# Optimization experiments

Hardware: AMD Instinct MI355X
Metric: run time of the kernel (lower is better)

The kernel has to match this reference:

```python
import jax, jax.numpy as jnp
import numpy as np

N = 100000   # nodes
E = 1600000  # edges (before self loops)
IN = 128     # input feature dim
H = 64       # hidden dim (single head GAT)
OUT = 2      # classifier output
NEG_SLOPE = 0.2


def setup_inputs() -> dict:
    key = jax.random.key(0)
    ks = jax.random.split(key, 14)
    s_in = 1.0 / np.sqrt(IN)
    s_h = 1.0 / np.sqrt(H)
    return {
        "x": jax.random.normal(ks[0], (N, IN), jnp.float32),
        "edge_index": jax.random.randint(ks[1], (2, E), 0, N, dtype=jnp.int64),
        # layer 0: in_ch -> hidden
        "W0": jax.random.normal(ks[2], (IN, H), jnp.float32) * s_in,
        "asrc0": jax.random.normal(ks[3], (H,), jnp.float32) * s_h,
        "adst0": jax.random.normal(ks[4], (H,), jnp.float32) * s_h,
        "b0": jnp.zeros((H,), jnp.float32),
        # layers 1..2: hidden -> hidden (stacked)
        "Ws": jax.random.normal(ks[5], (2, H, H), jnp.float32) * s_h,
        "asrcs": jax.random.normal(ks[6], (2, H), jnp.float32) * s_h,
        "adsts": jax.random.normal(ks[7], (2, H), jnp.float32) * s_h,
        "bs": jnp.zeros((2, H), jnp.float32),
        # classifier
        "Wc": jax.random.normal(ks[8], (H, OUT), jnp.float32) * s_h,
        "bc": jnp.zeros((OUT,), jnp.float32),
    }


def _gat_conv(x, W, a_src, a_dst, b, src, dst):
    """Single-head PyG GATConv (add_self_loops already applied to src/dst)."""
    h = x @ W                                   # [N, H]
    logit_s = h @ a_src                         # [N]
    logit_d = h @ a_dst                         # [N]
    e = jax.nn.leaky_relu(logit_s[src] + logit_d[dst], NEG_SLOPE)  # [E']
    # segment softmax over destination neighborhoods
    m = jax.ops.segment_max(e, dst, num_segments=N)                # [N]
    p = jnp.exp(e - m[dst])                                        # [E']
    denom = jax.ops.segment_sum(p, dst, num_segments=N)            # [N]
    alpha = p / (denom[dst] + 1e-16)                               # [E']
    out = jax.ops.segment_sum(alpha[:, None] * h[src], dst, num_segments=N)
    return out + b


def reference(x, edge_index, W0, asrc0, adst0, b0, Ws, asrcs, adsts, bs, Wc, bc):
    # PyG GATConv default add_self_loops=True
    loops = jnp.arange(N, dtype=edge_index.dtype)
    src = jnp.concatenate([edge_index[0], loops])
    dst = jnp.concatenate([edge_index[1], loops])

    h = jax.nn.relu(_gat_conv(x, W0, asrc0, adst0, b0, src, dst))
    for i in range(2):  # remaining num_layers-1 = 2 layers
        h = jax.nn.relu(_gat_conv(h, Ws[i], asrcs[i], adsts[i], bs[i], src, dst))
    # dropout is identity in eval mode
    return h @ Wc + bc
```

## Files before the change

kernel.cpp:

```cpp
#include <hip/hip_runtime.h>
#include <hip/hip_bf16.h>
#include <math.h>

#define NNODES 100000
#define NEDGES 1600000
#define EPLUS  (NEDGES + NNODES)
#define INF    128
#define HF     64
#define NEG_SLOPE 0.2f

#define CHUNK  4096
#define NCH    416
#define K1SH   10
#define NBK    98
#define HTLEN  (NBK * NCH)

__device__ __forceinline__ void edge_at(const int* __restrict__ ei, int i, int& s, int& d) {
    if (i < NEDGES) { s = ei[i]; d = ei[NEDGES + i]; } else { s = d = i - NEDGES; }
}

__global__ __launch_bounds__(256) void k_p1hist(const int* __restrict__ ei, int* __restrict__ hT) {
    __shared__ int h[NBK];
    const int c = blockIdx.x, t = threadIdx.x;
    if (t < NBK) h[t] = 0;
    __syncthreads();
    #pragma unroll
    for (int j = 0; j < CHUNK / 256; ++j) {
        int i = c * CHUNK + j * 256 + t;
        if (i < EPLUS) {
            int d = (i < NEDGES) ? ei[NEDGES + i] : (i - NEDGES);
            atomicAdd(&h[d >> K1SH], 1);
        }
    }
    __syncthreads();
    if (t < NBK) hT[t * NCH + c] = h[t];
}

__global__ __launch_bounds__(1024) void k_p2scan(int* __restrict__ hT, int* __restrict__ roff) {
    __shared__ int wsum[16], wpre[16];
    __shared__ int carry;
    const int t = threadIdx.x, lane = t & 63, w = t >> 6;
    if (t == 0) carry = 0;
    __syncthreads();
    const int len4 = HTLEN / 4;
    for (int base4 = 0; base4 < len4; base4 += 1024) {
        int idx4 = base4 + t;
        int4 a = make_int4(0, 0, 0, 0);
        if (idx4 < len4) a = ((const int4*)hT)[idx4];
        int s = a.x + a.y + a.z + a.w;
        int inc = s;
        #pragma unroll
        for (int o = 1; o < 64; o <<= 1) { int u = __shfl_up(inc, o); if (lane >= o) inc += u; }
        if (lane == 63) wsum[w] = inc;
        __syncthreads();
        if (t < 16) {
            int v = wsum[t], iv = v;
            #pragma unroll
            for (int o = 1; o < 16; o <<= 1) { int u = __shfl_up(iv, o); if (t >= o) iv += u; }
            wpre[t] = iv - v;
        }
        __syncthreads();
        int cl = carry;
        int excl = inc - s + wpre[w] + cl;
        if (idx4 < len4) {
            int4 e; e.x = excl; e.y = e.x + a.x; e.z = e.y + a.y; e.w = e.z + a.z;
            ((int4*)hT)[idx4] = e;
        }
        __syncthreads();
        if (t == 1023) carry = cl + wpre[15] + wsum[15];
        __syncthreads();
    }
    if (t == 0) roff[NNODES] = EPLUS;
}

__global__ __launch_bounds__(256) void k_p3part(const int* __restrict__ ei,
        const int* __restrict__ hT, int* __restrict__ pairs) {
    __shared__ int cur[NBK];
    const int c = blockIdx.x, t = threadIdx.x;
    if (t < NBK) cur[t] = hT[t * NCH + c];
    __syncthreads();
    #pragma unroll
    for (int j = 0; j < CHUNK / 256; ++j) {
        int i = c * CHUNK + j * 256 + t;
        if (i < EPLUS) {
            int s, d; edge_at(ei, i, s, d);
            int pos = atomicAdd(&cur[d >> K1SH], 1);
            pairs[pos] = (s << K1SH) | (d & 1023);
        }
    }
}

__global__ __launch_bounds__(512) void k_p4local(const int* __restrict__ hT,
        const int* __restrict__ pairs, int* __restrict__ roff, int* __restrict__ csr) {
    __shared__ int cnt[1024], woffl[1024];
    __shared__ int wsum[8], wpre[8];
    const int k = blockIdx.x, t = threadIdx.x, lane = t & 63, w = t >> 6;
    const int rstart = hT[k * NCH];
    const int rend   = (k + 1 < NBK) ? hT[(k + 1) * NCH] : EPLUS;
    cnt[t] = 0; cnt[t + 512] = 0;
    __syncthreads();
    for (int i = rstart + t; i < rend; i += 512) atomicAdd(&cnt[pairs[i] & 1023], 1);
    __syncthreads();
    int c0 = cnt[2 * t], c1 = cnt[2 * t + 1];
    int s = c0 + c1, inc = s;
    #pragma unroll
    for (int o = 1; o < 64; o <<= 1) { int u = __shfl_up(inc, o); if (lane >= o) inc += u; }
    if (lane == 63) wsum[w] = inc;
    __syncthreads();
    if (t < 8) {
        int v = wsum[t], iv = v;
        #pragma unroll
        for (int o = 1; o < 8; o <<= 1) { int u = __shfl_up(iv, o); if (t >= o) iv += u; }
        wpre[t] = iv - v;
    }
    __syncthreads();
    int excl = inc - s + wpre[w];
    woffl[2 * t] = excl; woffl[2 * t + 1] = excl + c0;
    int gn = (k << 10) + 2 * t;
    if (gn < NNODES)     roff[gn]     = rstart + excl;
    if (gn + 1 < NNODES) roff[gn + 1] = rstart + excl + c0;
    __syncthreads();
    for (int i = rstart + t; i < rend; i += 512) {
        int p = pairs[i];
        int lpos = atomicAdd(&woffl[p & 1023], 1);
        csr[rstart + lpos] = p >> K1SH;
    }
}

template<int IN>
__global__ __launch_bounds__(256) void k_transform(const float* __restrict__ X,
        const float* __restrict__ W, const float* __restrict__ asrc, const float* __restrict__ adst,
        float* __restrict__ H, float* __restrict__ ls, float* __restrict__ ld) {
    __shared__ float Wl[IN * HF];
    __shared__ float Xs[64 * 65];
    __shared__ float lssm[64], ldsm[64];
    const int t = threadIdx.x;
    for (int i = t * 4; i < IN * HF; i += 1024) *(float4*)&Wl[i] = *(const float4*)&W[i];

    const int nb = blockIdx.x * 64;
    const int nl = t & 63;
    const int f0 = (t >> 6) * 16;

    float acc[16] = {0.f,0.f,0.f,0.f,0.f,0.f,0.f,0.f,0.f,0.f,0.f,0.f,0.f,0.f,0.f,0.f};

    for (int kc = 0; kc < IN; kc += 64) {
        __syncthreads();
        #pragma unroll
        for (int it = 0; it < 4; ++it) {
            int i = t + it * 256;
            int r = i >> 4, c = i & 15;
            float4 xv = make_float4(0.f, 0.f, 0.f, 0.f);
            if (nb + r < NNODES) xv = *(const float4*)&X[(long long)(nb + r) * IN + kc + c * 4];
            Xs[r * 65 + c * 4 + 0] = xv.x;
            Xs[r * 65 + c * 4 + 1] = xv.y;
            Xs[r * 65 + c * 4 + 2] = xv.z;
            Xs[r * 65 + c * 4 + 3] = xv.w;
        }
        __syncthreads();
        #pragma unroll 4
        for (int k = 0; k < 64; ++k) {
            float xk = Xs[nl * 65 + k];
            #pragma unroll
            for (int f4 = 0; f4 < 4; ++f4) {
                float4 wv = *(const float4*)&Wl[(kc + k) * HF + f0 + f4 * 4];
                acc[f4 * 4 + 0] += xk * wv.x;
                acc[f4 * 4 + 1] += xk * wv.y;
                acc[f4 * 4 + 2] += xk * wv.z;
                acc[f4 * 4 + 3] += xk * wv.w;
            }
        }
    }

    if (t < 64) { lssm[t] = 0.f; ldsm[t] = 0.f; }
    __syncthreads();
    float hs = 0.f, hd = 0.f;
    #pragma unroll
    for (int f4 = 0; f4 < 4; ++f4) {
        float4 av = *(const float4*)&asrc[f0 + f4 * 4];
        float4 dv = *(const float4*)&adst[f0 + f4 * 4];
        hs += acc[f4*4+0]*av.x + acc[f4*4+1]*av.y + acc[f4*4+2]*av.z + acc[f4*4+3]*av.w;
        hd += acc[f4*4+0]*dv.x + acc[f4*4+1]*dv.y + acc[f4*4+2]*dv.z + acc[f4*4+3]*dv.w;
    }
    atomicAdd(&lssm[nl], hs);
    atomicAdd(&ldsm[nl], hd);
    if (nb + nl < NNODES) {
        #pragma unroll
        for (int f4 = 0; f4 < 4; ++f4)
            *(float4*)&H[(long long)(nb + nl) * HF + f0 + f4 * 4] =
                make_float4(acc[f4*4+0], acc[f4*4+1], acc[f4*4+2], acc[f4*4+3]);
    }
    __syncthreads();
    if (t < 64 && nb + t < NNODES) { ls[nb + t] = lssm[t]; ld[nb + t] = ldsm[t]; }
}

template<int FUSE_CLS>
__global__ __launch_bounds__(256) void k_gat(const int* __restrict__ roff, const int* __restrict__ csr,
        const float* __restrict__ ls, const float* __restrict__ ld, const float* __restrict__ H,
        const float* __restrict__ b, float* __restrict__ outX,
        const float* __restrict__ Wc, const float* __restrict__ bc, float* __restrict__ outC) {
    int n = blockIdx.x * 4 + (threadIdx.x >> 6);
    if (n >= NNODES) return;
    const int lane = threadIdx.x & 63;
    const int es = lane >> 4;
    const int fg = lane & 15;
    const int r0 = roff[n], r1 = roff[n + 1];
    const float ldv = ld[n];
    const float* __restrict__ Hf = H + fg * 4;
    float den = 0.f;
    float4 aA = make_float4(0.f,0.f,0.f,0.f), aB = make_float4(0.f,0.f,0.f,0.f);
    for (int base = r0; base < r1; base += 64) {
        const int nb = min(64, r1 - base);
        const bool ok = (lane < nb);
        int  sv = ok ? csr[base + lane] : 0;
        float e = ok ? (ls[sv] + ldv) : -INFINITY;
        e = e > 0.f ? e : NEG_SLOPE * e;
        float p  = __expf(e);
        float ts = p;
        #pragma unroll
        for (int o = 32; o; o >>= 1) ts += __shfl_xor(ts, o);
        den += ts;
        const int jmax = (nb + 3) >> 2;
        int j = 0;
        for (; j + 1 < jmax; j += 2) {
            int   j0 = j * 4 + es,      j1 = j0 + 4;
            int   s0 = __shfl(sv, j0),  s1 = __shfl(sv, j1);
            float p0 = __shfl(p,  j0),  p1 = __shfl(p,  j1);
            float4 h0 = *(const float4*)&Hf[(long long)s0 * HF];
            float4 h1 = *(const float4*)&Hf[(long long)s1 * HF];
            aA.x += p0 * h0.x; aA.y += p0 * h0.y; aA.z += p0 * h0.z; aA.w += p0 * h0.w;
            aB.x += p1 * h1.x; aB.y += p1 * h1.y; aB.z += p1 * h1.z; aB.w += p1 * h1.w;
        }
        if (j < jmax) {
            int   j0 = j * 4 + es;
            float p0 = __shfl(p,  j0);
            int   s0 = __shfl(sv, j0);
            if (p0 != 0.f) {
                float4 h0 = *(const float4*)&Hf[(long long)s0 * HF];
                aA.x += p0 * h0.x; aA.y += p0 * h0.y; aA.z += p0 * h0.z; aA.w += p0 * h0.w;
            }
        }
    }
    float4 acc = make_float4(aA.x + aB.x, aA.y + aB.y, aA.z + aB.z, aA.w + aB.w);
    #pragma unroll
    for (int o = 16; o <= 32; o <<= 1) {
        acc.x += __shfl_xor(acc.x, o);
        acc.y += __shfl_xor(acc.y, o);
        acc.z += __shfl_xor(acc.z, o);
        acc.w += __shfl_xor(acc.w, o);
    }
    const float inv = 1.f / (den + 1e-16f);
    const float4 bv = *(const float4*)&b[fg * 4];
    float4 v;
    v.x = fmaxf(acc.x * inv + bv.x, 0.f);
    v.y = fmaxf(acc.y * inv + bv.y, 0.f);
    v.z = fmaxf(acc.z * inv + bv.z, 0.f);
    v.w = fmaxf(acc.w * inv + bv.w, 0.f);
    if (!FUSE_CLS) {
        if (es == 0) *(float4*)&outX[(long long)n * HF + fg * 4] = v;
    } else {
        float a0 = 0.f, a1 = 0.f;
        if (es == 0) {
            a0 = v.x * Wc[(fg*4+0)*2+0] + v.y * Wc[(fg*4+1)*2+0] + v.z * Wc[(fg*4+2)*2+0] + v.w * Wc[(fg*4+3)*2+0];
            a1 = v.x * Wc[(fg*4+0)*2+1] + v.y * Wc[(fg*4+1)*2+1] + v.z * Wc[(fg*4+2)*2+1] + v.w * Wc[(fg*4+3)*2+1];
        }
        #pragma unroll
        for (int o = 32; o; o >>= 1) { a0 += __shfl_xor(a0, o); a1 += __shfl_xor(a1, o); }
        if (lane == 0) { outC[n * 2 + 0] = a0 + bc[0]; outC[n * 2 + 1] = a1 + bc[1]; }
    }
}

extern "C" void kernel_launch(void* const* d_in, const int* in_sizes, int n_in,
                              void* d_out, int out_size, void* d_ws, size_t ws_size,
                              hipStream_t stream) {
    const float* x      = (const float*)d_in[0];
    const int*   ei     = (const int*)d_in[1];
    const float* W0     = (const float*)d_in[2];
    const float* asrc0  = (const float*)d_in[3];
    const float* adst0  = (const float*)d_in[4];
    const float* b0     = (const float*)d_in[5];
    const float* Ws     = (const float*)d_in[6];
    const float* asrcs  = (const float*)d_in[7];
    const float* adsts  = (const float*)d_in[8];
    const float* bs     = (const float*)d_in[9];
    const float* Wc     = (const float*)d_in[10];
    const float* bc     = (const float*)d_in[11];
    float* out = (float*)d_out;

    float* Hb   = (float*)d_ws;
    float* P    = Hb + (long long)NNODES * HF;
    float* ls   = P + (long long)NNODES * HF;
    float* ld   = ls + NNODES;
    int* roff   = (int*)(ld + NNODES);
    int* hT     = roff + NNODES + 4;
    int* csr    = hT + HTLEN;
    int* pairs  = csr + EPLUS;

    const int B = 256;
    const int gNode4 = (NNODES + 3) / 4;
    const int gT     = (NNODES + 63) / 64;

    k_p1hist<<<NCH, B, 0, stream>>>(ei, hT);
    k_p2scan<<<1, 1024, 0, stream>>>(hT, roff);
    k_p3part<<<NCH, B, 0, stream>>>(ei, hT, pairs);
    k_p4local<<<NBK, 512, 0, stream>>>(hT, pairs, roff, csr);

    k_transform<INF><<<gT, B, 0, stream>>>(x, W0, asrc0, adst0, Hb, ls, ld);
    k_gat<0><<<gNode4, B, 0, stream>>>(roff, csr, ls, ld, Hb, b0, P, nullptr, nullptr, nullptr);

    k_transform<HF><<<gT, B, 0, stream>>>(P, Ws + 0 * HF * HF, asrcs + 0 * HF, adsts + 0 * HF, P, ls, ld);
    k_gat<0><<<gNode4, B, 0, stream>>>(roff, csr, ls, ld, P, bs + 0 * HF, Hb, nullptr, nullptr, nullptr);

    k_transform<HF><<<gT, B, 0, stream>>>(Hb, Ws + 1 * HF * HF, asrcs + 1 * HF, adsts + 1 * HF, Hb, ls, ld);
    k_gat<1><<<gNode4, B, 0, stream>>>(roff, csr, ls, ld, Hb, bs + 1 * HF, nullptr, Wc, bc, out);
}
```

Before: 353.0 us.

## Precompute per-edge attention weights in a separate edge-parallel kernel

Measured after the change: 401.5 us. 13.7% more time.

```diff
diff --git a/kernel.cpp b/kernel.cpp
--- a/kernel.cpp
+++ b/kernel.cpp
@@ -91,7 +91,8 @@
 }
 
 __global__ __launch_bounds__(512) void k_p4local(const int* __restrict__ hT,
-        const int* __restrict__ pairs, int* __restrict__ roff, int* __restrict__ csr) {
+        const int* __restrict__ pairs, int* __restrict__ roff, int* __restrict__ csr,
+        int* __restrict__ dstarr) {
     __shared__ int cnt[1024], woffl[1024];
     __shared__ int wsum[8], wpre[8];
     const int k = blockIdx.x, t = threadIdx.x, lane = t & 63, w = t >> 6;
@@ -123,7 +124,30 @@
     for (int i = rstart + t; i < rend; i += 512) {
         int p = pairs[i];
         int lpos = atomicAdd(&woffl[p & 1023], 1);
-        csr[rstart + lpos] = p >> K1SH;
+        csr[rstart + lpos]    = p >> K1SH;
+        dstarr[rstart + lpos] = (k << K1SH) | (p & 1023);
+    }
+}
+
+__global__ __launch_bounds__(256) void k_prep(const int* __restrict__ csr,
+        const int* __restrict__ dstarr, const float* __restrict__ ls,
+        const float* __restrict__ ld, float* __restrict__ pe) {
+    int i4 = blockIdx.x * blockDim.x + threadIdx.x;
+    int i = i4 * 4;
+    if (i + 3 < EPLUS) {
+        int4 sv = *(const int4*)&csr[i];
+        int4 dv = *(const int4*)&dstarr[i];
+        float4 r;
+        float e0 = ls[sv.x] + ld[dv.x]; r.x = __expf(e0 > 0.f ? e0 : NEG_SLOPE * e0);
+        float e1 = ls[sv.y] + ld[dv.y]; r.y = __expf(e1 > 0.f ? e1 : NEG_SLOPE * e1);
+        float e2 = ls[sv.z] + ld[dv.z]; r.z = __expf(e2 > 0.f ? e2 : NEG_SLOPE * e2);
+        float e3 = ls[sv.w] + ld[dv.w]; r.w = __expf(e3 > 0.f ? e3 : NEG_SLOPE * e3);
+        *(float4*)&pe[i] = r;
+    } else {
+        for (; i < EPLUS; ++i) {
+            float e = ls[csr[i]] + ld[dstarr[i]];
+            pe[i] = __expf(e > 0.f ? e : NEG_SLOPE * e);
+        }
     }
 }
 
@@ -195,7 +219,7 @@
 
 template<int FUSE_CLS>
 __global__ __launch_bounds__(256) void k_gat(const int* __restrict__ roff, const int* __restrict__ csr,
-        const float* __restrict__ ls, const float* __restrict__ ld, const float* __restrict__ H,
+        const float* __restrict__ pe, const float* __restrict__ H,
         const float* __restrict__ b, float* __restrict__ outX,
         const float* __restrict__ Wc, const float* __restrict__ bc, float* __restrict__ outC) {
     int n = blockIdx.x * 4 + (threadIdx.x >> 6);
@@ -204,42 +228,30 @@
     const int es = lane >> 4;
     const int fg = lane & 15;
     const int r0 = roff[n], r1 = roff[n + 1];
-    const float ldv = ld[n];
     const float* __restrict__ Hf = H + fg * 4;
+
     float den = 0.f;
+    for (int i = r0 + lane; i < r1; i += 64) den += pe[i];
+
     float4 aA = make_float4(0.f,0.f,0.f,0.f), aB = make_float4(0.f,0.f,0.f,0.f);
-    for (int base = r0; base < r1; base += 64) {
-        const int nb = min(64, r1 - base);
-        const bool ok = (lane < nb);
-        int  sv = ok ? csr[base + lane] : 0;
-        float e = ok ? (ls[sv] + ldv) : -INFINITY;
-        e = e > 0.f ? e : NEG_SLOPE * e;
-        float p  = __expf(e);
-        float ts = p;
-        #pragma unroll
-        for (int o = 32; o; o >>= 1) ts += __shfl_xor(ts, o);
-        den += ts;
-        const int jmax = (nb + 3) >> 2;
-        int j = 0;
-        for (; j + 1 < jmax; j += 2) {
-            int   j0 = j * 4 + es,      j1 = j0 + 4;
-            int   s0 = __shfl(sv, j0),  s1 = __shfl(sv, j1);
-            float p0 = __shfl(p,  j0),  p1 = __shfl(p,  j1);
-            float4 h0 = *(const float4*)&Hf[(long long)s0 * HF];
-            float4 h1 = *(const float4*)&Hf[(long long)s1 * HF];
-            aA.x += p0 * h0.x; aA.y += p0 * h0.y; aA.z += p0 * h0.z; aA.w += p0 * h0.w;
-            aB.x += p1 * h1.x; aB.y += p1 * h1.y; aB.z += p1 * h1.z; aB.w += p1 * h1.w;
-        }
-        if (j < jmax) {
-            int   j0 = j * 4 + es;
-            float p0 = __shfl(p,  j0);
-            int   s0 = __shfl(sv, j0);
-            if (p0 != 0.f) {
-                float4 h0 = *(const float4*)&Hf[(long long)s0 * HF];
-                aA.x += p0 * h0.x; aA.y += p0 * h0.y; aA.z += p0 * h0.z; aA.w += p0 * h0.w;
-            }
-        }
-    }
+    int i = r0 + es;
+    for (; i + 4 < r1; i += 8) {
+        int   s0 = csr[i];     int   s1 = csr[i + 4];
+        float p0 = pe[i];      float p1 = pe[i + 4];
+        float4 h0 = *(const float4*)&Hf[(long long)s0 * HF];
+        float4 h1 = *(const float4*)&Hf[(long long)s1 * HF];
+        aA.x += p0 * h0.x; aA.y += p0 * h0.y; aA.z += p0 * h0.z; aA.w += p0 * h0.w;
+        aB.x += p1 * h1.x; aB.y += p1 * h1.y; aB.z += p1 * h1.z; aB.w += p1 * h1.w;
+    }
+    if (i < r1) {
+        int   s0 = csr[i];
+        float p0 = pe[i];
+        float4 h0 = *(const float4*)&Hf[(long long)s0 * HF];
+        aA.x += p0 * h0.x; aA.y += p0 * h0.y; aA.z += p0 * h0.z; aA.w += p0 * h0.w;
+    }
+
+    #pragma unroll
+    for (int o = 1; o < 64; o <<= 1) den += __shfl_xor(den, o);
     float4 acc = make_float4(aA.x + aB.x, aA.y + aB.y, aA.z + aB.z, aA.w + aB.w);
     #pragma unroll
     for (int o = 16; o <= 32; o <<= 1) {
@@ -286,30 +298,36 @@
     const float* bc     = (const float*)d_in[11];
     float* out = (float*)d_out;
 
-    float* Hb   = (float*)d_ws;
-    float* P    = Hb + (long long)NNODES * HF;
-    float* ls   = P + (long long)NNODES * HF;
-    float* ld   = ls + NNODES;
-    int* roff   = (int*)(ld + NNODES);
-    int* hT     = roff + NNODES + 4;
-    int* csr    = hT + HTLEN;
-    int* pairs  = csr + EPLUS;
+    float* Hb     = (float*)d_ws;
+    float* P      = Hb + (long long)NNODES * HF;
+    float* ls     = P + (long long)NNODES * HF;
+    float* ld     = ls + NNODES;
+    int*   roff   = (int*)(ld + NNODES);
+    int*   hT     = roff + NNODES + 4;
+    int*   csr    = hT + HTLEN;
+    int*   pairs  = csr + EPLUS;
+    int*   dstarr = pairs + EPLUS;
+    float* pe     = (float*)(dstarr + EPLUS);
 
     const int B = 256;
     const int gNode4 = (NNODES + 3) / 4;
     const int gT     = (NNODES + 63) / 64;
+    const int gPrep  = (EPLUS / 4 + B - 1) / B;
 
     k_p1hist<<<NCH, B, 0, stream>>>(ei, hT);
     k_p2scan<<<1, 1024, 0, stream>>>(hT, roff);
     k_p3part<<<NCH, B, 0, stream>>>(ei, hT, pairs);
-    k_p4local<<<NBK, 512, 0, stream>>>(hT, pairs, roff, csr);
+    k_p4local<<<NBK, 512, 0, stream>>>(hT, pairs, roff, csr, dstarr);
 
     k_transform<INF><<<gT, B, 0, stream>>>(x, W0, asrc0, adst0, Hb, ls, ld);
-    k_gat<0><<<gNode4, B, 0, stream>>>(roff, csr, ls, ld, Hb, b0, P, nullptr, nullptr, nullptr);
+    k_prep<<<gPrep, B, 0, stream>>>(csr, dstarr, ls, ld, pe);
+    k_gat<0><<<gNode4, B, 0, stream>>>(roff, csr, pe, Hb, b0, P, nullptr, nullptr, nullptr);
 
     k_transform<HF><<<gT, B, 0, stream>>>(P, Ws + 0 * HF * HF, asrcs + 0 * HF, adsts + 0 * HF, P, ls, ld);
-    k_gat<0><<<gNode4, B, 0, stream>>>(roff, csr, ls, ld, P, bs + 0 * HF, Hb, nullptr, nullptr, nullptr);
+    k_prep<<<gPrep, B, 0, stream>>>(csr, dstarr, ls, ld, pe);
+    k_gat<0><<<gNode4, B, 0, stream>>>(roff, csr, pe, P, bs + 0 * HF, Hb, nullptr, nullptr, nullptr);
 
     k_transform<HF><<<gT, B, 0, stream>>>(Hb, Ws + 1 * HF * HF, asrcs + 1 * HF, adsts + 1 * HF, Hb, ls, ld);
-    k_gat<1><<<gNode4, B, 0, stream>>>(roff, csr, ls, ld, Hb, bs + 1 * HF, nullptr, Wc, bc, out);
-}
+    k_prep<<<gPrep, B, 0, stream>>>(csr, dstarr, ls, ld, pe);
+    k_gat<1><<<gNode4, B, 0, stream>>>(roff, csr, pe, Hb, bs + 1 * HF, nullptr, Wc, bc, out);
+}
```

## Split GAT aggregation into four feature slices per node with interleaved block mapping

Applied to the files above, without the earlier changes.

Result: slower. 593.8 us (+68.2%).

```diff
diff --git a/kernel.cpp b/kernel.cpp
--- a/kernel.cpp
+++ b/kernel.cpp
@@ -193,80 +193,79 @@
     if (t < 64 && nb + t < NNODES) { ls[nb + t] = lssm[t]; ld[nb + t] = ldsm[t]; }
 }
 
-template<int FUSE_CLS>
-__global__ __launch_bounds__(256) void k_gat(const int* __restrict__ roff, const int* __restrict__ csr,
-        const float* __restrict__ ls, const float* __restrict__ ld, const float* __restrict__ H,
-        const float* __restrict__ b, float* __restrict__ outX,
-        const float* __restrict__ Wc, const float* __restrict__ bc, float* __restrict__ outC) {
-    int n = blockIdx.x * 4 + (threadIdx.x >> 6);
+__global__ __launch_bounds__(256) void k_gat_slice(const int* __restrict__ roff,
+        const int* __restrict__ csr, const float* __restrict__ ls, const float* __restrict__ ld,
+        const float* __restrict__ H, const float* __restrict__ b, float* __restrict__ outX) {
+    const int bid  = blockIdx.x;
+    const int wv   = threadIdx.x >> 6;
+    const int lane = threadIdx.x & 63;
+    const int es   = lane >> 2;
+    const int fl   = lane & 3;
+    const int grp  = (bid >> 3) * 2 + (bid & 1);
+    const int slice = (bid & 7) >> 1;
+    const int n = grp * 4 + wv;
     if (n >= NNODES) return;
-    const int lane = threadIdx.x & 63;
-    const int es = lane >> 4;
-    const int fg = lane & 15;
     const int r0 = roff[n], r1 = roff[n + 1];
     const float ldv = ld[n];
-    const float* __restrict__ Hf = H + fg * 4;
+    const float* __restrict__ Hs = H + slice * 16 + fl * 4;
+
     float den = 0.f;
     float4 aA = make_float4(0.f,0.f,0.f,0.f), aB = make_float4(0.f,0.f,0.f,0.f);
-    for (int base = r0; base < r1; base += 64) {
-        const int nb = min(64, r1 - base);
-        const bool ok = (lane < nb);
-        int  sv = ok ? csr[base + lane] : 0;
-        float e = ok ? (ls[sv] + ldv) : -INFINITY;
-        e = e > 0.f ? e : NEG_SLOPE * e;
-        float p  = __expf(e);
-        float ts = p;
-        #pragma unroll
-        for (int o = 32; o; o >>= 1) ts += __shfl_xor(ts, o);
-        den += ts;
-        const int jmax = (nb + 3) >> 2;
-        int j = 0;
-        for (; j + 1 < jmax; j += 2) {
-            int   j0 = j * 4 + es,      j1 = j0 + 4;
-            int   s0 = __shfl(sv, j0),  s1 = __shfl(sv, j1);
-            float p0 = __shfl(p,  j0),  p1 = __shfl(p,  j1);
-            float4 h0 = *(const float4*)&Hf[(long long)s0 * HF];
-            float4 h1 = *(const float4*)&Hf[(long long)s1 * HF];
-            aA.x += p0 * h0.x; aA.y += p0 * h0.y; aA.z += p0 * h0.z; aA.w += p0 * h0.w;
-            aB.x += p1 * h1.x; aB.y += p1 * h1.y; aB.z += p1 * h1.z; aB.w += p1 * h1.w;
-        }
-        if (j < jmax) {
-            int   j0 = j * 4 + es;
-            float p0 = __shfl(p,  j0);
-            int   s0 = __shfl(sv, j0);
-            if (p0 != 0.f) {
-                float4 h0 = *(const float4*)&Hf[(long long)s0 * HF];
-                aA.x += p0 * h0.x; aA.y += p0 * h0.y; aA.z += p0 * h0.z; aA.w += p0 * h0.w;
-            }
-        }
-    }
+    int i = r0 + es;
+    for (; i + 16 < r1; i += 32) {
+        int   s0 = csr[i];         int   s1 = csr[i + 16];
+        float e0 = ls[s0] + ldv;   float e1 = ls[s1] + ldv;
+        e0 = e0 > 0.f ? e0 : NEG_SLOPE * e0;
+        e1 = e1 > 0.f ? e1 : NEG_SLOPE * e1;
+        float p0 = __expf(e0), p1 = __expf(e1);
+        den += p0 + p1;
+        float4 h0 = *(const float4*)&Hs[(long long)s0 * HF];
+        float4 h1 = *(const float4*)&Hs[(long long)s1 * HF];
+        aA.x += p0 * h0.x; aA.y += p0 * h0.y; aA.z += p0 * h0.z; aA.w += p0 * h0.w;
+        aB.x += p1 * h1.x; aB.y += p1 * h1.y; aB.z += p1 * h1.z; aB.w += p1 * h1.w;
+    }
+    if (i < r1) {
+        int   s0 = csr[i];
+        float e0 = ls[s0] + ldv;
+        e0 = e0 > 0.f ? e0 : NEG_SLOPE * e0;
+        float p0 = __expf(e0);
+        den += p0;
+        float4 h0 = *(const float4*)&Hs[(long long)s0 * HF];
+        aA.x += p0 * h0.x; aA.y += p0 * h0.y; aA.z += p0 * h0.z; aA.w += p0 * h0.w;
+    }
+
     float4 acc = make_float4(aA.x + aB.x, aA.y + aB.y, aA.z + aB.z, aA.w + aB.w);
     #pragma unroll
-    for (int o = 16; o <= 32; o <<= 1) {
+    for (int o = 4; o <= 32; o <<= 1) {
+        den   += __shfl_xor(den,   o);
         acc.x += __shfl_xor(acc.x, o);
         acc.y += __shfl_xor(acc.y, o);
         acc.z += __shfl_xor(acc.z, o);
         acc.w += __shfl_xor(acc.w, o);
     }
     const float inv = 1.f / (den + 1e-16f);
-    const float4 bv = *(const float4*)&b[fg * 4];
-    float4 v;
-    v.x = fmaxf(acc.x * inv + bv.x, 0.f);
-    v.y = fmaxf(acc.y * inv + bv.y, 0.f);
-    v.z = fmaxf(acc.z * inv + bv.z, 0.f);
-    v.w = fmaxf(acc.w * inv + bv.w, 0.f);
-    if (!FUSE_CLS) {
-        if (es == 0) *(float4*)&outX[(long long)n * HF + fg * 4] = v;
-    } else {
-        float a0 = 0.f, a1 = 0.f;
-        if (es == 0) {
-            a0 = v.x * Wc[(fg*4+0)*2+0] + v.y * Wc[(fg*4+1)*2+0] + v.z * Wc[(fg*4+2)*2+0] + v.w * Wc[(fg*4+3)*2+0];
-            a1 = v.x * Wc[(fg*4+0)*2+1] + v.y * Wc[(fg*4+1)*2+1] + v.z * Wc[(fg*4+2)*2+1] + v.w * Wc[(fg*4+3)*2+1];
-        }
-        #pragma unroll
-        for (int o = 32; o; o >>= 1) { a0 += __shfl_xor(a0, o); a1 += __shfl_xor(a1, o); }
-        if (lane == 0) { outC[n * 2 + 0] = a0 + bc[0]; outC[n * 2 + 1] = a1 + bc[1]; }
-    }
+    if (es == 0) {
+        const float4 bv = *(const float4*)&b[slice * 16 + fl * 4];
+        float4 v;
+        v.x = fmaxf(acc.x * inv + bv.x, 0.f);
+        v.y = fmaxf(acc.y * inv + bv.y, 0.f);
+        v.z = fmaxf(acc.z * inv + bv.z, 0.f);
+        v.w = fmaxf(acc.w * inv + bv.w, 0.f);
+        *(float4*)&outX[(long long)n * HF + slice * 16 + fl * 4] = v;
+    }
+}
+
+__global__ __launch_bounds__(256) void k_cls(const float* __restrict__ X,
+        const float* __restrict__ Wc, const float* __restrict__ bc, float* __restrict__ out) {
+    long long n = (long long)blockIdx.x * 4 + (threadIdx.x >> 6);
+    if (n >= NNODES) return;
+    const int lane = threadIdx.x & 63;
+    float v = X[n * HF + lane];
+    float r0 = v * Wc[lane * 2 + 0];
+    float r1 = v * Wc[lane * 2 + 1];
+    #pragma unroll
+    for (int o = 32; o; o >>= 1) { r0 += __shfl_xor(r0, o); r1 += __shfl_xor(r1, o); }
+    if (lane == 0) { out[n * 2 + 0] = r0 + bc[0]; out[n * 2 + 1] = r1 + bc[1]; }
 }
 
 extern "C" void kernel_launch(void* const* d_in, const int* in_sizes, int n_in,
@@ -296,8 +295,9 @@
     int* pairs  = csr + EPLUS;
 
     const int B = 256;
+    const int gT     = (NNODES + 63) / 64;
+    const int gSlice = 100000;
     const int gNode4 = (NNODES + 3) / 4;
-    const int gT     = (NNODES + 63) / 64;
 
     k_p1hist<<<NCH, B, 0, stream>>>(ei, hT);
     k_p2scan<<<1, 1024, 0, stream>>>(hT, roff);
@@ -305,11 +305,12 @@
     k_p4local<<<NBK, 512, 0, stream>>>(hT, pairs, roff, csr);
 
     k_transform<INF><<<gT, B, 0, stream>>>(x, W0, asrc0, adst0, Hb, ls, ld);
-    k_gat<0><<<gNode4, B, 0, stream>>>(roff, csr, ls, ld, Hb, b0, P, nullptr, nullptr, nullptr);
+    k_gat_slice<<<gSlice, B, 0, stream>>>(roff, csr, ls, ld, Hb, b0, P);
 
     k_transform<HF><<<gT, B, 0, stream>>>(P, Ws + 0 * HF * HF, asrcs + 0 * HF, adsts + 0 * HF, P, ls, ld);
-    k_gat<0><<<gNode4, B, 0, stream>>>(roff, csr, ls, ld, P, bs + 0 * HF, Hb, nullptr, nullptr, nullptr);
+    k_gat_slice<<<gSlice, B, 0, stream>>>(roff, csr, ls, ld, P, bs + 0 * HF, Hb);
 
     k_transform<HF><<<gT, B, 0, stream>>>(Hb, Ws + 1 * HF * HF, asrcs + 1 * HF, adsts + 1 * HF, Hb, ls, ld);
-    k_gat<1><<<gNode4, B, 0, stream>>>(roff, csr, ls, ld, Hb, bs + 1 * HF, nullptr, Wc, bc, out);
-}
+    k_gat_slice<<<gSlice, B, 0, stream>>>(roff, csr, ls, ld, Hb, bs + 1 * HF, P);
+    k_cls<<<gNode4, B, 0, stream>>>(P, Wc, bc, out);
+}
```
